# Optimization experiments

Hardware: AMD Instinct MI355X
Metric: run time of the kernel (lower is better)

## Reference

```python
import jax, jax.numpy as jnp
import numpy as np

NUM_TASKS, IN_SIZE, OUT_SIZE, N_ROWS = 64, 512, 512, 2048


def setup_inputs() -> dict:
    key = jax.random.key(0)
    k_x, k_t, k_w = jax.random.split(key, 3)
    inputs = jax.random.normal(k_x, (N_ROWS, IN_SIZE), dtype=jnp.float32)
    task_ids = jax.random.randint(k_t, (N_ROWS,), 0, NUM_TASKS, dtype=jnp.int64)
    # in_size == out_size path: identity + N(0, 0.03) perturbation per task
    W = (jnp.eye(IN_SIZE, OUT_SIZE, dtype=jnp.float32)[None]
         + 0.03 * jax.random.normal(k_w, (NUM_TASKS, IN_SIZE, OUT_SIZE), dtype=jnp.float32))
    return {"inputs": inputs, "task_ids": task_ids, "W": W}


def reference(inputs, task_ids, W):
    # Gather the full per-row weight matrix then batched vector-matrix multiply,
    # faithful to torch.einsum('ni,nio->no', inputs, W[task_ids]).
    aligned = W[task_ids]                       # [I, in, out]
    return jnp.einsum("ni,nio->no", inputs, aligned)  # [I, out]
```

## Files before the change

### kernel.cpp

```cpp
#include <hip/hip_runtime.h>


#define NDIM 512
#define KDIM 512
#define NCOL 32
#define KCH  256

typedef _Float16 f16x8 __attribute__((ext_vector_type(8)));
typedef float    f32x4 __attribute__((ext_vector_type(4)));

__global__ __launch_bounds__(256) void k_rowlist(
    const int* __restrict__ tids, int* __restrict__ cnt,
    int* __restrict__ rows, int n_rows)
{
    __shared__ int lc[64];
    const int tid = threadIdx.x;
    if (tid < 64) lc[tid] = 0;
    __syncthreads();
    for (int i = tid; i < n_rows; i += 256) {
        const int t = tids[i];
        const int p = atomicAdd(&lc[t], 1);
        rows[t * 2048 + p] = i;
    }
    __syncthreads();
    if (tid < 64) cnt[tid] = lc[tid];
}

__global__ __launch_bounds__(256) void k_gemm(
    const float* __restrict__ x, const float* __restrict__ W,
    const int* __restrict__ cnt, const int* __restrict__ rows,
    float* __restrict__ out)
{
    const int tid  = threadIdx.x;
    const int lane = tid & 63;
    const int wv   = tid >> 6;
    const int c0   = blockIdx.x * NCOL;
    const int task = blockIdx.y;

    const int count = cnt[task];
    if (count == 0) return;

    __shared__ __align__(16) _Float16 Wt[NCOL * KCH];

    const int ml = lane & 15;
    const int q  = lane >> 4;
    const float* Wg = W + (size_t)task * KDIM * NDIM + c0;
    const int*   rl = rows + task * 2048;

    const int sc4  = (tid & 7) * 4;
    const int soct = tid >> 3;

    for (int g0 = 0; g0 < count; g0 += 64) {
        const int rr = g0 + wv * 16 + ml;
        const int rowid = rl[(rr < count) ? rr : 0];
        const float* xrow = x + (size_t)rowid * KDIM;

        f32x4 acc[2] = {};

        #pragma unroll
        for (int kc = 0; kc < 2; ++kc) {
            const int kb = kc * KCH;

            float4 wr[8];
            #pragma unroll
            for (int j = 0; j < 8; ++j)
                wr[j] = *(const float4*)(Wg + (size_t)(kb + soct * 8 + j) * NDIM + sc4);
            #pragma unroll
            for (int j2 = 0; j2 < 4; ++j2) {
                f16x8 h;
                #pragma unroll
                for (int j = 0; j < 8; ++j)
                    h[j] = (_Float16)(((const float*)&wr[j])[j2]);
                const int c  = sc4 + j2;
                const int po = soct ^ (c & 7);
                *(f16x8*)(&Wt[c * KCH + po * 8]) = h;
            }

            float4 xa[16];
            #pragma unroll
            for (int ks = 0; ks < 8; ++ks) {
                xa[2 * ks]     = *(const float4*)(xrow + kb + ks * 32 + q * 8);
                xa[2 * ks + 1] = *(const float4*)(xrow + kb + ks * 32 + q * 8 + 4);
            }

            __syncthreads();

            #pragma unroll
            for (int ks = 0; ks < 8; ++ks) {
                const float4 a0 = xa[2 * ks];
                const float4 a1 = xa[2 * ks + 1];
                f16x8 af;
                af[0] = (_Float16)a0.x; af[1] = (_Float16)a0.y;
                af[2] = (_Float16)a0.z; af[3] = (_Float16)a0.w;
                af[4] = (_Float16)a1.x; af[5] = (_Float16)a1.y;
                af[6] = (_Float16)a1.z; af[7] = (_Float16)a1.w;
                #pragma unroll
                for (int ct = 0; ct < 2; ++ct) {
                    const int cB = ct * 16 + ml;
                    const int po = (ks * 4 + q) ^ (cB & 7);
                    const f16x8 bf = *(const f16x8*)(&Wt[cB * KCH + po * 8]);
                    acc[ct] = __builtin_amdgcn_mfma_f32_16x16x32_f16(af, bf, acc[ct], 0, 0, 0);
                }
            }
            __syncthreads();
        }

        #pragma unroll
        for (int rg = 0; rg < 4; ++rg) {
            const int rr2 = g0 + wv * 16 + q * 4 + rg;
            if (rr2 < count) {
                float* op = out + (size_t)rl[rr2] * NDIM + c0 + ml;
                op[0]  = acc[0][rg];
                op[16] = acc[1][rg];
            }
        }
    }
}

extern "C" void kernel_launch(void* const* d_in, const int* in_sizes, int n_in,
                              void* d_out, int out_size, void* d_ws, size_t ws_size,
                              hipStream_t stream) {
    const float* x    = (const float*)d_in[0];
    const int*   tids = (const int*)d_in[1];
    const float* W    = (const float*)d_in[2];
    float*       out  = (float*)d_out;
    const int n_rows  = in_sizes[1];

    int* cnt  = (int*)d_ws;
    int* rows = (int*)d_ws + 64;

    k_rowlist<<<dim3(1), dim3(256), 0, stream>>>(tids, cnt, rows, n_rows);
    k_gemm<<<dim3(NDIM / NCOL, 64), dim3(256), 0, stream>>>(x, W, cnt, rows, out);
}
```

Measured before the change: 112.6 us.

## Fuse task row-list construction into GEMM kernel and stage full-K weights once

Removes the separate single-block row-list kernel. Each GEMM block now scans task_ids itself with wave ballots to build its own row list in shared memory. All 512 K rows of the block's weight slice are loaded into LDS once before the row loop, instead of being reloaded per 64-row group and K-half, which also removes the per-chunk barriers. The weight loads are issued before the ballot scan so they overlap it. The cost is that every block redundantly reads all 2048 task ids, uses more LDS, and silently assumes at most 128 rows per wave slice and 256 rows per task.

```diff
diff --git a/kernel.cpp b/kernel.cpp
--- a/kernel.cpp
+++ b/kernel.cpp
@@ -4,32 +4,16 @@
 #define NDIM 512
 #define KDIM 512
 #define NCOL 32
-#define KCH  256
 
 typedef _Float16 f16x8 __attribute__((ext_vector_type(8)));
 typedef float    f32x4 __attribute__((ext_vector_type(4)));
 
-__global__ __launch_bounds__(256) void k_rowlist(
-    const int* __restrict__ tids, int* __restrict__ cnt,
-    int* __restrict__ rows, int n_rows)
-{
-    __shared__ int lc[64];
-    const int tid = threadIdx.x;
-    if (tid < 64) lc[tid] = 0;
-    __syncthreads();
-    for (int i = tid; i < n_rows; i += 256) {
-        const int t = tids[i];
-        const int p = atomicAdd(&lc[t], 1);
-        rows[t * 2048 + p] = i;
-    }
-    __syncthreads();
-    if (tid < 64) cnt[tid] = lc[tid];
-}
-
-__global__ __launch_bounds__(256) void k_gemm(
-    const float* __restrict__ x, const float* __restrict__ W,
-    const int* __restrict__ cnt, const int* __restrict__ rows,
-    float* __restrict__ out)
+__global__ __launch_bounds__(256) void k_fused(
+    const float* __restrict__ x,
+    const int*   __restrict__ tids,
+    const float* __restrict__ W,
+    float*       __restrict__ out,
+    int n_rows)
 {
     const int tid  = threadIdx.x;
     const int lane = tid & 63;
@@ -37,18 +21,74 @@
     const int c0   = blockIdx.x * NCOL;
     const int task = blockIdx.y;
 
-    const int count = cnt[task];
+    __shared__ __align__(16) _Float16 Wt[NCOL * KDIM];
+    __shared__ unsigned short rlw[4 * 128];
+    __shared__ unsigned short rl[256];
+    __shared__ int wcnt[4];
+
+    int trow[8], tval[8];
+    #pragma unroll
+    for (int it = 0; it < 8; ++it) {
+        trow[it] = wv * 512 + it * 64 + lane;
+        tval[it] = (trow[it] < n_rows) ? tids[trow[it]] : -1;
+    }
+
+    const int sc4   = (tid & 7) * 4;
+    const int obase = tid >> 3;
+    const float* Wg = W + (size_t)task * KDIM * NDIM + c0;
+    float4 wr[16];
+    #pragma unroll
+    for (int j = 0; j < 8; ++j)
+        wr[j] = *(const float4*)(Wg + (size_t)(obase * 8 + j) * NDIM + sc4);
+    #pragma unroll
+    for (int j = 0; j < 8; ++j)
+        wr[8 + j] = *(const float4*)(Wg + (size_t)((obase + 32) * 8 + j) * NDIM + sc4);
+
+    int cloc = 0;
+    #pragma unroll
+    for (int it = 0; it < 8; ++it) {
+        const bool m = (tval[it] == task);
+        const unsigned long long bal = __ballot(m);
+        const int rank = __popcll(bal & ((1ull << lane) - 1ull));
+        if (m) rlw[wv * 128 + cloc + rank] = (unsigned short)trow[it];
+        cloc += __popcll(bal);
+    }
+    if (lane == 0) wcnt[wv] = cloc;
+
+    #pragma unroll
+    for (int h = 0; h < 2; ++h) {
+        const int oct = obase + h * 32;
+        #pragma unroll
+        for (int j2 = 0; j2 < 4; ++j2) {
+            f16x8 h8;
+            #pragma unroll
+            for (int j = 0; j < 8; ++j)
+                h8[j] = (_Float16)(((const float*)&wr[h * 8 + j])[j2]);
+            const int c  = sc4 + j2;
+            const int po = oct ^ (c & 7);
+            *(f16x8*)&Wt[c * KDIM + po * 8] = h8;
+        }
+    }
+
+    __syncthreads();
+
+    const int n0 = wcnt[0], n1 = wcnt[1], n2 = wcnt[2], n3 = wcnt[3];
+    const int o1 = n0, o2 = n0 + n1, o3 = o2 + n2;
+    const int count = o3 + n3;
+    if (tid < count && tid < 256) {
+        int w, base;
+        if (tid < o1)      { w = 0; base = 0;  }
+        else if (tid < o2) { w = 1; base = o1; }
+        else if (tid < o3) { w = 2; base = o2; }
+        else               { w = 3; base = o3; }
+        rl[tid] = rlw[w * 128 + tid - base];
+    }
+    __syncthreads();
+
     if (count == 0) return;
-
-    __shared__ __align__(16) _Float16 Wt[NCOL * KCH];
 
     const int ml = lane & 15;
     const int q  = lane >> 4;
-    const float* Wg = W + (size_t)task * KDIM * NDIM + c0;
-    const int*   rl = rows + task * 2048;
-
-    const int sc4  = (tid & 7) * 4;
-    const int soct = tid >> 3;
 
     for (int g0 = 0; g0 < count; g0 += 64) {
         const int rr = g0 + wv * 16 + ml;
@@ -56,53 +96,29 @@
         const float* xrow = x + (size_t)rowid * KDIM;
 
         f32x4 acc[2] = {};
-
         #pragma unroll
-        for (int kc = 0; kc < 2; ++kc) {
-            const int kb = kc * KCH;
-
-            float4 wr[8];
-            #pragma unroll
-            for (int j = 0; j < 8; ++j)
-                wr[j] = *(const float4*)(Wg + (size_t)(kb + soct * 8 + j) * NDIM + sc4);
-            #pragma unroll
-            for (int j2 = 0; j2 < 4; ++j2) {
-                f16x8 h;
-                #pragma unroll
-                for (int j = 0; j < 8; ++j)
-                    h[j] = (_Float16)(((const float*)&wr[j])[j2]);
-                const int c  = sc4 + j2;
-                const int po = soct ^ (c & 7);
-                *(f16x8*)(&Wt[c * KCH + po * 8]) = h;
-            }
-
+        for (int p = 0; p < 2; ++p) {
+            const int kb = p * 256;
             float4 xa[16];
             #pragma unroll
             for (int ks = 0; ks < 8; ++ks) {
                 xa[2 * ks]     = *(const float4*)(xrow + kb + ks * 32 + q * 8);
                 xa[2 * ks + 1] = *(const float4*)(xrow + kb + ks * 32 + q * 8 + 4);
             }
-
-            __syncthreads();
-
             #pragma unroll
             for (int ks = 0; ks < 8; ++ks) {
-                const float4 a0 = xa[2 * ks];
-                const float4 a1 = xa[2 * ks + 1];
                 f16x8 af;
-                af[0] = (_Float16)a0.x; af[1] = (_Float16)a0.y;
-                af[2] = (_Float16)a0.z; af[3] = (_Float16)a0.w;
-                af[4] = (_Float16)a1.x; af[5] = (_Float16)a1.y;
-                af[6] = (_Float16)a1.z; af[7] = (_Float16)a1.w;
+                const float* a0 = (const float*)&xa[2 * ks];
+                #pragma unroll
+                for (int j = 0; j < 8; ++j) af[j] = (_Float16)a0[j];
                 #pragma unroll
                 for (int ct = 0; ct < 2; ++ct) {
                     const int cB = ct * 16 + ml;
-                    const int po = (ks * 4 + q) ^ (cB & 7);
-                    const f16x8 bf = *(const f16x8*)(&Wt[cB * KCH + po * 8]);
+                    const int po = (p * 32 + ks * 4 + q) ^ (cB & 7);
+                    const f16x8 bf = *(const f16x8*)&Wt[cB * KDIM + po * 8];
                     acc[ct] = __builtin_amdgcn_mfma_f32_16x16x32_f16(af, bf, acc[ct], 0, 0, 0);
                 }
             }
-            __syncthreads();
         }
 
         #pragma unroll
@@ -126,9 +142,5 @@
     float*       out  = (float*)d_out;
     const int n_rows  = in_sizes[1];
 
-    int* cnt  = (int*)d_ws;
-    int* rows = (int*)d_ws + 64;
-
-    k_rowlist<<<dim3(1), dim3(256), 0, stream>>>(tids, cnt, rows, n_rows);
-    k_gemm<<<dim3(NDIM / NCOL, 64), dim3(256), 0, stream>>>(x, W, cnt, rows, out);
+    k_fused<<<dim3(NDIM / NCOL, 64), dim3(256), 0, stream>>>(x, tids, W, out, n_rows);
 }
```

New measurement: 108.0 us. 1.04x faster.
